# Kernel tuning notes

Measured on AMD Instinct MI355X. Metric: run time of the kernel, lower is better.

## Reference

```python
import jax, jax.numpy as jnp
import numpy as np

B, H, L, D = 2, 16, 2048, 64


def setup_inputs() -> dict:
    key = jax.random.key(0)
    kq, kk, kv = jax.random.split(key, 3)
    queries = jax.random.normal(kq, (B, H, L, D), dtype=jnp.float32)
    keys = jax.random.normal(kk, (B, H, L, D), dtype=jnp.float32)
    values = jax.random.normal(kv, (B, H, L, D), dtype=jnp.float32)
    # causal mask: True = masked (as consumed by masked_fill in the original)
    attn_mask = jnp.triu(jnp.ones((L, L), dtype=bool), k=1)
    return {"queries": queries, "keys": keys, "values": values, "attn_mask": attn_mask}


def reference(queries, keys, values, attn_mask):
    D_ = queries.shape[-1]
    scale = 1.0 / jnp.sqrt(jnp.asarray(D_, dtype=queries.dtype))
    # [B,H,Lq,Lk] score matrix (faithfully materialized as in the original)
    scores = jnp.einsum("bhqd,bhkd->bhqk", queries, keys) * scale
    scores = jnp.where(attn_mask, jnp.asarray(-1e9, dtype=scores.dtype), scores)
    attention = jax.nn.softmax(scores, axis=-1)
    # dropout rate = 0.0 (inference); identity
    out = jnp.einsum("bhqk,bhkd->bhqd", attention, values)
    return out
```

## Files before the change

### kernel.cpp

```cpp
#include <hip/hip_runtime.h>


constexpr int Lq = 2048;
constexpr int Dh = 64;
constexpr int QB = 64;
constexpr int KV = 64;
constexpr int TILEB = 16384;
constexpr int VOFF  = 8192;

typedef __attribute__((ext_vector_type(16))) float f32x16;
typedef __attribute__((ext_vector_type(4))) float f32x4;
typedef __attribute__((ext_vector_type(8))) unsigned short u16x8;
typedef __attribute__((ext_vector_type(4))) unsigned int u32x4;
typedef __attribute__((ext_vector_type(8))) __bf16 bf16x8;

__device__ __forceinline__ unsigned short f2bf(float f) {
  __bf16 h = (__bf16)f;
  return __builtin_bit_cast(unsigned short, h);
}
__device__ __forceinline__ unsigned pack2(float a, float b) {
  return (unsigned)f2bf(a) | ((unsigned)f2bf(b) << 16);
}
__device__ __forceinline__ f32x16 mfma32(u16x8 a, u16x8 b, f32x16 c) {
  return __builtin_amdgcn_mfma_f32_32x32x16_bf16(
      __builtin_bit_cast(bf16x8, a), __builtin_bit_cast(bf16x8, b), c, 0, 0, 0);
}
__device__ __forceinline__ void plswap(unsigned a, unsigned b,
                                       unsigned& wlo, unsigned& whi) {
#if __has_builtin(__builtin_amdgcn_permlane32_swap)
  auto r = __builtin_amdgcn_permlane32_swap((int)a, (int)b, false, false);
  wlo = (unsigned)r[0];
  whi = (unsigned)r[1];
#else
  const int hh = (threadIdx.x >> 5) & 1;
  unsigned pa = (unsigned)__shfl_xor((int)a, 32);
  unsigned pb = (unsigned)__shfl_xor((int)b, 32);
  wlo = hh ? pb : a;
  whi = hh ? b : pa;
#endif
}

__global__ __launch_bounds__(256, 2)
void repack(const float* __restrict__ K, const float* __restrict__ V,
            unsigned char* __restrict__ W) {
  __shared__ unsigned short Vl[64][72];

  const int tid = threadIdx.x;
  const int bt  = blockIdx.x;
  const int bh  = bt >> 5;
  const int tl  = bt & 31;
  const size_t src = (size_t)bh * Lq * Dh + (size_t)tl * KV * Dh;
  unsigned char* img = W + (size_t)bt * TILEB;

  const int r  = tid >> 2;
  const int c2 = (tid & 3) * 2;

  {
    const float* kp = K + src + (size_t)r * Dh + c2 * 8;
    f32x4 a = *(const f32x4*)kp;
    f32x4 b = *(const f32x4*)(kp + 4);
    f32x4 c = *(const f32x4*)(kp + 8);
    f32x4 d = *(const f32x4*)(kp + 12);
    u16x8 lo, hi;
    #pragma unroll
    for (int j = 0; j < 4; ++j) {
      lo[j] = f2bf(a[j]); lo[4 + j] = f2bf(b[j]);
      hi[j] = f2bf(c[j]); hi[4 + j] = f2bf(d[j]);
    }
    *(u16x8*)(img + (c2 * 64 + r) * 16)       = lo;
    *(u16x8*)(img + ((c2 + 1) * 64 + r) * 16) = hi;
  }
  {
    const float* vp = V + src + (size_t)r * Dh + c2 * 8;
    f32x4 a = *(const f32x4*)vp;
    f32x4 b = *(const f32x4*)(vp + 4);
    f32x4 c = *(const f32x4*)(vp + 8);
    f32x4 d = *(const f32x4*)(vp + 12);
    u16x8 lo, hi;
    #pragma unroll
    for (int j = 0; j < 4; ++j) {
      lo[j] = f2bf(a[j]); lo[4 + j] = f2bf(b[j]);
      hi[j] = f2bf(c[j]); hi[4 + j] = f2bf(d[j]);
    }
    *(u16x8*)&Vl[r][c2 * 8]     = lo;
    *(u16x8*)&Vl[r][c2 * 8 + 8] = hi;
  }
  __syncthreads();
  {
    u16x8 lo, hi;
    #pragma unroll
    for (int e = 0; e < 8; ++e) {
      lo[e] = Vl[c2 * 8 + e][r];
      hi[e] = Vl[c2 * 8 + 8 + e][r];
    }
    *(u16x8*)(img + VOFF + (c2 * 64 + r) * 16)       = lo;
    *(u16x8*)(img + VOFF + ((c2 + 1) * 64 + r) * 16) = hi;
  }
}

__global__ __launch_bounds__(256, 3)
void fattn_fwd(const float* __restrict__ Q, const unsigned char* __restrict__ W,
               float* __restrict__ O) {
  __shared__ float Mrg[2][64][33];

  const int tid  = threadIdx.x;
  const int lane = tid & 63;
  const int w    = tid >> 6;
  const int l31  = lane & 31;
  const int h    = lane >> 5;
  const int qg   = w >> 1;
  const int kh   = w & 1;

  const int bid = blockIdx.x;
  const int xcd = bid & 7;
  const int s_  = bid >> 3;
  const int u   = s_ & 31;
  const int k   = s_ >> 5;
  const int bh  = xcd * 4 + k;
  const int qt  = (k & 1) ? u : (31 - u);
  const int qb  = qt * QB;
  const size_t base = (size_t)bh * Lq * Dh;

  u16x8 qc[4];
  {
    const float* qp = Q + base + (size_t)(qb + qg * 32 + l31) * Dh + h * 8;
    #pragma unroll
    for (int dc = 0; dc < 4; ++dc) {
      f32x4 lo = *(const f32x4*)(qp + dc * 16);
      f32x4 hi = *(const f32x4*)(qp + dc * 16 + 4);
      u16x8 f;
      #pragma unroll
      for (int j = 0; j < 4; ++j) { f[j] = f2bf(lo[j]); f[4 + j] = f2bf(hi[j]); }
      qc[dc] = f;
    }
  }

  const int qmin   = qb + qg * 32;
  const int lastkv = qmin + 31 - kh * 32;
  const int nw     = (lastkv >= 0) ? (lastkv >> 6) + 1 : 0;

  const unsigned char* Wb = W + (size_t)(bh * 32) * TILEB;

  f32x16 accO0, accO1;
  #pragma unroll
  for (int i = 0; i < 16; ++i) { accO0[i] = 0.f; accO1[i] = 0.f; }
  float ls0 = 0.f, ls1 = 0.f, ls2 = 0.f, ls3 = 0.f;

  const float C1 = 0.125f * 1.4426950408889634f;
  const float C0 = -10.0f * 1.4426950408889634f;

  auto ldK = [&](u16x8 (&kf)[4], int t) {
    const unsigned char* p = Wb + (size_t)t * TILEB + (kh * 32 + l31) * 16;
    #pragma unroll
    for (int dc = 0; dc < 4; ++dc)
      kf[dc] = *(const u16x8*)(p + (dc * 2 + h) * 1024);
  };
  auto ldV = [&](u16x8 (&vf)[4], int t) {
    const unsigned char* p =
        Wb + (size_t)t * TILEB + VOFF + (kh * 4 + h) * 1024 + l31 * 16;
    #pragma unroll
    for (int c2 = 0; c2 < 2; ++c2) {
      vf[c2 * 2 + 0] = *(const u16x8*)(p + c2 * 2048);
      vf[c2 * 2 + 1] = *(const u16x8*)(p + c2 * 2048 + 512);
    }
  };

  auto compute = [&](u16x8 (&kf)[4], u16x8 (&vf)[4], int t) {
    const int kv0 = t * 64 + kh * 32;
    f32x16 s;
    #pragma unroll
    for (int i = 0; i < 16; ++i) s[i] = 0.f;
    __builtin_amdgcn_s_setprio(1);
    #pragma unroll
    for (int dc = 0; dc < 4; ++dc) s = mfma32(kf[dc], qc[dc], s);
    __builtin_amdgcn_s_setprio(0);

    float p[16];
    if (kv0 + 31 > qmin) {
      const int qrow = qmin + l31;
      #pragma unroll
      for (int r = 0; r < 16; ++r) {
        float e = __builtin_amdgcn_exp2f(s[r] * C1 + C0);
        const int kvg = kv0 + (r & 3) + 8 * (r >> 2) + 4 * h;
        p[r] = (kvg <= qrow) ? e : 0.0f;
      }
    } else {
      #pragma unroll
      for (int r = 0; r < 16; ++r)
        p[r] = __builtin_amdgcn_exp2f(s[r] * C1 + C0);
    }
    ls0 += (p[0] + p[1]) + (p[2] + p[3]);
    ls1 += (p[4] + p[5]) + (p[6] + p[7]);
    ls2 += (p[8] + p[9]) + (p[10] + p[11]);
    ls3 += (p[12] + p[13]) + (p[14] + p[15]);

    unsigned pk[4][2];
    #pragma unroll
    for (int q4 = 0; q4 < 4; ++q4) {
      pk[q4][0] = pack2(p[q4 * 4 + 0], p[q4 * 4 + 1]);
      pk[q4][1] = pack2(p[q4 * 4 + 2], p[q4 * 4 + 3]);
    }
    __builtin_amdgcn_s_setprio(1);
    #pragma unroll
    for (int c2 = 0; c2 < 2; ++c2) {
      unsigned w0, w1, w2, w3;
      plswap(pk[2 * c2][0], pk[2 * c2 + 1][0], w0, w2);
      plswap(pk[2 * c2][1], pk[2 * c2 + 1][1], w1, w3);
      u32x4 pw = {w0, w1, w2, w3};
      u16x8 pf = __builtin_bit_cast(u16x8, pw);
      accO0 = mfma32(vf[c2 * 2 + 0], pf, accO0);
      accO1 = mfma32(vf[c2 * 2 + 1], pf, accO1);
    }
    __builtin_amdgcn_s_setprio(0);
  };

  if (nw > 0) {
    u16x8 kA[4], kB[4], vv[4];
    ldK(kA, 0);
    int t = 0;
    while (t + 2 <= nw) {
      ldK(kB, t + 1);
      ldV(vv, t);
      compute(kA, vv, t);
      const int tn = (t + 2 < nw) ? (t + 2) : (nw - 1);
      ldK(kA, tn);
      ldV(vv, t + 1);
      compute(kB, vv, t + 1);
      t += 2;
    }
    if (t < nw) {
      ldV(vv, t);
      compute(kA, vv, t);
    }
  }

  const float lsum = (ls0 + ls1) + (ls2 + ls3);
  __syncthreads();
  if (kh == 1) {
    float* m = &Mrg[qg][lane][0];
    #pragma unroll
    for (int r = 0; r < 16; ++r) { m[r] = accO0[r]; m[16 + r] = accO1[r]; }
    m[32] = lsum;
  }
  __syncthreads();
  if (kh == 0) {
    const float* m = &Mrg[qg][lane][0];
    float ls = lsum + m[32];
    ls += __shfl_xor(ls, 32);
    const float inv = 1.0f / ls;
    float* op = O + base + (size_t)(qb + qg * 32 + l31) * Dh;
    #pragma unroll
    for (int r = 0; r < 16; ++r) {
      const int d = (r & 3) + 8 * (r >> 2) + 4 * h;
      op[d]      = (accO0[r] + m[r]) * inv;
      op[32 + d] = (accO1[r] + m[16 + r]) * inv;
    }
  }
}

extern "C" void kernel_launch(void* const* d_in, const int* in_sizes, int n_in,
                              void* d_out, int out_size, void* d_ws, size_t ws_size,
                              hipStream_t stream) {
  const float* Q = (const float*)d_in[0];
  const float* K = (const float*)d_in[1];
  const float* V = (const float*)d_in[2];
  float* O = (float*)d_out;
  unsigned char* W = (unsigned char*)d_ws;

  repack<<<dim3(1024), dim3(256), 0, stream>>>(K, V, W);
  fattn_fwd<<<dim3(1024), dim3(256), 0, stream>>>(Q, W, O);
}
```

Baseline: 52.18 us.

## Reorder QK MFMA before loads, use packed bf16 convert, raise occupancy bound

Splits the per-tile compute into a QK step and a softmax/PV step, and issues the QK MFMAs before the next K/V global loads so matrix work overlaps with memory latency. Tile addressing moves from per-call index arithmetic to an incrementing pointer with precomputed lane offsets, and the final-iteration redundant K reload is skipped. The bf16 packing uses the v_cvt_pk_bf16_f32 instruction instead of two scalar conversions. Launch bounds move from 3 to 4 blocks per CU, which tightens the register budget and may cause spills.

```diff
diff --git a/kernel.cpp b/kernel.cpp
--- a/kernel.cpp
+++ b/kernel.cpp
@@ -4,7 +4,6 @@
 constexpr int Lq = 2048;
 constexpr int Dh = 64;
 constexpr int QB = 64;
-constexpr int KV = 64;
 constexpr int TILEB = 16384;
 constexpr int VOFF  = 8192;
 
@@ -18,8 +17,10 @@
   __bf16 h = (__bf16)f;
   return __builtin_bit_cast(unsigned short, h);
 }
-__device__ __forceinline__ unsigned pack2(float a, float b) {
-  return (unsigned)f2bf(a) | ((unsigned)f2bf(b) << 16);
+__device__ __forceinline__ unsigned cvtpk(float lo, float hi) {
+  unsigned r;
+  asm("v_cvt_pk_bf16_f32 %0, %1, %2" : "=v"(r) : "v"(lo), "v"(hi));
+  return r;
 }
 __device__ __forceinline__ f32x16 mfma32(u16x8 a, u16x8 b, f32x16 c) {
   return __builtin_amdgcn_mfma_f32_32x32x16_bf16(
@@ -49,7 +50,7 @@
   const int bt  = blockIdx.x;
   const int bh  = bt >> 5;
   const int tl  = bt & 31;
-  const size_t src = (size_t)bh * Lq * Dh + (size_t)tl * KV * Dh;
+  const size_t src = (size_t)bh * Lq * Dh + (size_t)tl * 64 * Dh;
   unsigned char* img = W + (size_t)bt * TILEB;
 
   const int r  = tid >> 2;
@@ -98,7 +99,7 @@
   }
 }
 
-__global__ __launch_bounds__(256, 3)
+__global__ __launch_bounds__(256, 4)
 void fattn_fwd(const float* __restrict__ Q, const unsigned char* __restrict__ W,
                float* __restrict__ O) {
   __shared__ float Mrg[2][64][33];
@@ -138,8 +139,7 @@
   const int qmin   = qb + qg * 32;
   const int lastkv = qmin + 31 - kh * 32;
   const int nw     = (lastkv >= 0) ? (lastkv >> 6) + 1 : 0;
-
-  const unsigned char* Wb = W + (size_t)(bh * 32) * TILEB;
+  const int kvh    = kh * 32;
 
   f32x16 accO0, accO1;
   #pragma unroll
@@ -149,24 +149,25 @@
   const float C1 = 0.125f * 1.4426950408889634f;
   const float C0 = -10.0f * 1.4426950408889634f;
 
-  auto ldK = [&](u16x8 (&kf)[4], int t) {
-    const unsigned char* p = Wb + (size_t)t * TILEB + (kh * 32 + l31) * 16;
-    #pragma unroll
-    for (int dc = 0; dc < 4; ++dc)
-      kf[dc] = *(const u16x8*)(p + (dc * 2 + h) * 1024);
-  };
-  auto ldV = [&](u16x8 (&vf)[4], int t) {
-    const unsigned char* p =
-        Wb + (size_t)t * TILEB + VOFF + (kh * 4 + h) * 1024 + l31 * 16;
-    #pragma unroll
-    for (int c2 = 0; c2 < 2; ++c2) {
-      vf[c2 * 2 + 0] = *(const u16x8*)(p + c2 * 2048);
-      vf[c2 * 2 + 1] = *(const u16x8*)(p + c2 * 2048 + 512);
-    }
-  };
-
-  auto compute = [&](u16x8 (&kf)[4], u16x8 (&vf)[4], int t) {
-    const int kv0 = t * 64 + kh * 32;
+  const int laneK = (kvh + l31) * 16 + h * 1024;
+  const int laneV = VOFF + (kh * 4 + h) * 1024 + l31 * 16;
+
+  auto ldK = [&](u16x8 (&kf)[4], const unsigned char* pT) {
+    const unsigned char* p = pT + laneK;
+    kf[0] = *(const u16x8*)(p);
+    kf[1] = *(const u16x8*)(p + 2048);
+    kf[2] = *(const u16x8*)(p + 4096);
+    kf[3] = *(const u16x8*)(p + 6144);
+  };
+  auto ldV = [&](u16x8 (&vf)[4], const unsigned char* pT) {
+    const unsigned char* p = pT + laneV;
+    vf[0] = *(const u16x8*)(p);
+    vf[1] = *(const u16x8*)(p + 512);
+    vf[2] = *(const u16x8*)(p + 2048);
+    vf[3] = *(const u16x8*)(p + 2560);
+  };
+
+  auto qk = [&](const u16x8 (&kf)[4]) -> f32x16 {
     f32x16 s;
     #pragma unroll
     for (int i = 0; i < 16; ++i) s[i] = 0.f;
@@ -174,7 +175,10 @@
     #pragma unroll
     for (int dc = 0; dc < 4; ++dc) s = mfma32(kf[dc], qc[dc], s);
     __builtin_amdgcn_s_setprio(0);
-
+    return s;
+  };
+
+  auto spv = [&](const f32x16& s, const u16x8 (&vf)[4], int kv0) {
     float p[16];
     if (kv0 + 31 > qmin) {
       const int qrow = qmin + l31;
@@ -197,8 +201,8 @@
     unsigned pk[4][2];
     #pragma unroll
     for (int q4 = 0; q4 < 4; ++q4) {
-      pk[q4][0] = pack2(p[q4 * 4 + 0], p[q4 * 4 + 1]);
-      pk[q4][1] = pack2(p[q4 * 4 + 2], p[q4 * 4 + 3]);
+      pk[q4][0] = cvtpk(p[q4 * 4 + 0], p[q4 * 4 + 1]);
+      pk[q4][1] = cvtpk(p[q4 * 4 + 2], p[q4 * 4 + 3]);
     }
     __builtin_amdgcn_s_setprio(1);
     #pragma unroll
@@ -215,22 +219,28 @@
   };
 
   if (nw > 0) {
+    const unsigned char* pT = W + (size_t)(bh * 32) * TILEB;
     u16x8 kA[4], kB[4], vv[4];
-    ldK(kA, 0);
+    ldK(kA, pT);
     int t = 0;
+    int kv0 = kvh;
     while (t + 2 <= nw) {
-      ldK(kB, t + 1);
-      ldV(vv, t);
-      compute(kA, vv, t);
-      const int tn = (t + 2 < nw) ? (t + 2) : (nw - 1);
-      ldK(kA, tn);
-      ldV(vv, t + 1);
-      compute(kB, vv, t + 1);
-      t += 2;
+      f32x16 s = qk(kA);
+      ldK(kB, pT + TILEB);
+      ldV(vv, pT);
+      spv(s, vv, kv0);
+
+      s = qk(kB);
+      if (t + 2 < nw) ldK(kA, pT + 2 * TILEB);
+      ldV(vv, pT + TILEB);
+      spv(s, vv, kv0 + 64);
+
+      t += 2; pT += 2 * TILEB; kv0 += 128;
     }
     if (t < nw) {
-      ldV(vv, t);
-      compute(kA, vv, t);
+      f32x16 s = qk(kA);
+      ldV(vv, pT);
+      spv(s, vv, kv0);
     }
   }
 
```

Result: slower. 98.14 us (+88.1%).
